# Kernel optimization log

Hardware: AMD Instinct MI355X
Metric: run time of the kernel (lower is better)

Reference implementation:

```python
import jax, jax.numpy as jnp
import numpy as np

N_NODES = 50000


def _sage_conv(x, src, dst, W_l, b_l, W_r):
    # PyG SAGEConv (aggr='mean'): out = lin_l(mean_{j in N(i)} x_j) + lin_r(x_i)
    # lin_l has bias, lin_r has no bias.
    neigh_sum = jax.ops.segment_sum(x[src], dst, num_segments=N_NODES)  # [N, F]
    deg = jax.ops.segment_sum(jnp.ones_like(dst, dtype=x.dtype), dst, num_segments=N_NODES)
    neigh_mean = neigh_sum / jnp.maximum(deg, 1.0)[:, None]
    return neigh_mean @ W_l.T + b_l + x @ W_r.T


def setup_inputs() -> dict:
    key = jax.random.key(0)
    ks = jax.random.split(key, 8)
    D, H, C = 768, 128, 4
    x = jax.random.normal(ks[0], (N_NODES, D), dtype=jnp.float32)
    edge_index = jax.random.randint(ks[1], (2, 800000), 0, N_NODES, dtype=jnp.int64)
    s1 = 1.0 / np.sqrt(D)
    s2 = 1.0 / np.sqrt(H)
    return {
        "x": x,
        "edge_index": edge_index,
        "W1_l": jax.random.uniform(ks[2], (H, D), jnp.float32, -s1, s1),
        "b1_l": jnp.zeros((H,), jnp.float32),
        "W1_r": jax.random.uniform(ks[3], (H, D), jnp.float32, -s1, s1),
        "W2_l": jax.random.uniform(ks[4], (C, H), jnp.float32, -s2, s2),
        "b2_l": jnp.zeros((C,), jnp.float32),
        "W2_r": jax.random.uniform(ks[5], (C, H), jnp.float32, -s2, s2),
    }


def reference(x, edge_index, W1_l, b1_l, W1_r, W2_l, b2_l, W2_r):
    src, dst = edge_index[0], edge_index[1]
    h = jax.nn.relu(_sage_conv(x, src, dst, W1_l, b1_l, W1_r))  # [N, H]
    out = _sage_conv(h, src, dst, W2_l, b2_l, W2_r)  # [N, C]
    return out
```

## Files before the change

### kernel.cpp

```cpp
#include <hip/hip_runtime.h>


typedef __bf16 bf16x8 __attribute__((ext_vector_type(8)));
typedef float  f32x4  __attribute__((ext_vector_type(4)));

__device__ __forceinline__ float bf16_lo(uint32_t w) {
    union { uint32_t u; float f; } c; c.u = w << 16; return c.f;
}
__device__ __forceinline__ float bf16_hi(uint32_t w) {
    union { uint32_t u; float f; } c; c.u = w & 0xffff0000u; return c.f;
}

__global__ __launch_bounds__(256)
void prep(const float* __restrict__ W1l, const float* __restrict__ W1r,
          __bf16* __restrict__ Bp, int* __restrict__ deg, int N)
{
    int i = blockIdx.x * 256 + threadIdx.x;
    if (i < N) deg[i] = 0;
    if (i < 256 * 768) {
        int col = i / 768, k = i - col * 768;
        float v = (col < 128) ? W1l[col * 768 + k] : W1r[(col - 128) * 768 + k];
        Bp[((k >> 3) << 11) + (col << 3) + (k & 7)] = (__bf16)v;
    }
}

__global__ __launch_bounds__(256)
void csr_count(const int* __restrict__ ei, int* __restrict__ deg, int E)
{
    int e = blockIdx.x * 256 + threadIdx.x;
    if (e >= E) return;
    atomicAdd(&deg[ei[E + e]], 1);
}

__global__ __launch_bounds__(1024)
void scan1(const int* __restrict__ deg, int* __restrict__ row_ptr,
           int* __restrict__ partials, int N)
{
    __shared__ int buf[1024];
    int i = blockIdx.x * 1024 + threadIdx.x;
    int v = (i < N) ? deg[i] : 0;
    int val = v;
    buf[threadIdx.x] = val;
    __syncthreads();
    for (int off = 1; off < 1024; off <<= 1) {
        int t = (threadIdx.x >= (unsigned)off) ? buf[threadIdx.x - off] : 0;
        __syncthreads();
        val += t;
        buf[threadIdx.x] = val;
        __syncthreads();
    }
    if (i < N) row_ptr[i] = val - v;
    if (threadIdx.x == 1023) partials[blockIdx.x] = val;
}

__global__ __launch_bounds__(1024)
void scan23(int* __restrict__ row_ptr, int* __restrict__ cursor,
            const int* __restrict__ partials, int N, int E, int nb)
{
    __shared__ int soff;
    int b = blockIdx.x;
    if (threadIdx.x < 64) {
        int lane = threadIdx.x;
        int v = (lane < nb) ? partials[lane] : 0;
        int s = v;
        #pragma unroll
        for (int off = 1; off < 64; off <<= 1) {
            int t = __shfl_up(s, off);
            if (lane >= off) s += t;
        }
        if (lane == b) soff = s - v;
    }
    __syncthreads();
    int off = soff;
    int i = b * 1024 + threadIdx.x;
    if (i < N) {
        int v = row_ptr[i] + off;
        row_ptr[i] = v;
        cursor[i]  = v;
    }
    if (b == 0 && threadIdx.x == 0) row_ptr[N] = E;
}

__global__ __launch_bounds__(512)
void gemm_fill(const float* __restrict__ A, const __bf16* __restrict__ Bp,
               __bf16* __restrict__ Cb, int M, int mtiles,
               const int* __restrict__ ei, int* __restrict__ cursor,
               int* __restrict__ csr_src, int E)
{
    constexpr int LDK = 136;
    __shared__ __bf16 As[64][LDK];
    const int tid = threadIdx.x;

    if ((int)blockIdx.x >= mtiles) {
        int stride = (gridDim.x - mtiles) * 512;
        for (int e = (blockIdx.x - mtiles) * 512 + tid; e < E; e += stride) {
            int src = ei[e];
            int dst = ei[E + e];
            int pos = atomicAdd(&cursor[dst], 1);
            csr_src[pos] = src;
        }
        return;
    }

    const int bm   = blockIdx.x * 64;
    const int lane = tid & 63;
    const int wave = tid >> 6;
    const int wr = wave >> 2, wc = wave & 3;
    const int l15 = lane & 15;
    const int lk  = lane >> 4;

    f32x4 acc[2][4] = {};
    float4 apref[4];

    const int arow = tid >> 3;
    const int akc  = (tid & 7) << 4;
    const __bf16* bbase = Bp + ((size_t)(wc * 64 + l15) << 3) + ((size_t)lk << 11);

    auto load_A = [&](int k0) {
        if (bm + arow < M) {
            const float* src = A + (size_t)(bm + arow) * 768 + k0 + akc;
            apref[0] = *(const float4*)src;
            apref[1] = *(const float4*)(src + 4);
            apref[2] = *(const float4*)(src + 8);
            apref[3] = *(const float4*)(src + 12);
        } else {
            apref[0] = apref[1] = apref[2] = apref[3] = make_float4(0.f, 0.f, 0.f, 0.f);
        }
    };

    load_A(0);
    for (int kt = 0; kt < 6; ++kt) {
        if (kt) __syncthreads();
        {
            bf16x8 b0, b1;
            b0[0] = (__bf16)apref[0].x; b0[1] = (__bf16)apref[0].y;
            b0[2] = (__bf16)apref[0].z; b0[3] = (__bf16)apref[0].w;
            b0[4] = (__bf16)apref[1].x; b0[5] = (__bf16)apref[1].y;
            b0[6] = (__bf16)apref[1].z; b0[7] = (__bf16)apref[1].w;
            b1[0] = (__bf16)apref[2].x; b1[1] = (__bf16)apref[2].y;
            b1[2] = (__bf16)apref[2].z; b1[3] = (__bf16)apref[2].w;
            b1[4] = (__bf16)apref[3].x; b1[5] = (__bf16)apref[3].y;
            b1[6] = (__bf16)apref[3].z; b1[7] = (__bf16)apref[3].w;
            *(bf16x8*)&As[arow][akc]     = b0;
            *(bf16x8*)&As[arow][akc + 8] = b1;
        }
        __syncthreads();
        if (kt < 5) load_A((kt + 1) * 128);

        #pragma unroll
        for (int ksp = 0; ksp < 2; ++ksp) {
            bf16x8 bcur[2][4];
            #pragma unroll
            for (int k2 = 0; k2 < 2; ++k2)
                #pragma unroll
                for (int j = 0; j < 4; ++j)
                    bcur[k2][j] = *(const bf16x8*)(bbase +
                        (((size_t)(kt * 16 + (ksp * 2 + k2) * 4) << 11) +
                         ((size_t)j << 7)));
            #pragma unroll
            for (int k2 = 0; k2 < 2; ++k2) {
                int koff = (ksp * 2 + k2) * 32 + lk * 8;
                bf16x8 af[2];
                #pragma unroll
                for (int i = 0; i < 2; ++i)
                    af[i] = *(const bf16x8*)&As[wr * 32 + i * 16 + l15][koff];
                #pragma unroll
                for (int i = 0; i < 2; ++i)
                    #pragma unroll
                    for (int j = 0; j < 4; ++j)
                        acc[i][j] = __builtin_amdgcn_mfma_f32_16x16x32_bf16(
                            af[i], bcur[k2][j], acc[i][j], 0, 0, 0);
            }
        }
    }

    #pragma unroll
    for (int i = 0; i < 2; ++i)
        #pragma unroll
        for (int j = 0; j < 4; ++j)
            #pragma unroll
            for (int v = 0; v < 4; ++v) {
                int row = bm + wr * 32 + i * 16 + lk * 4 + v;
                int col = wc * 64 + j * 16 + l15;
                if (row < M) Cb[(size_t)row * 256 + col] = (__bf16)acc[i][j][v];
            }
}

__global__ __launch_bounds__(256)
void sage1_fused(const int* __restrict__ row_ptr, const int* __restrict__ csr_src,
                 const __bf16* __restrict__ pq, const float* __restrict__ b1,
                 const float* __restrict__ W2l, const float* __restrict__ W2r,
                 float* __restrict__ r, float* __restrict__ s, int N)
{
    __shared__ float Wl[512], Wr[512];
    for (int i = threadIdx.x; i < 512; i += 256) {
        Wl[i] = W2l[i];
        Wr[i] = W2r[i];
    }
    __syncthreads();

    int wid  = threadIdx.x >> 6;
    int lane = threadIdx.x & 63;
    int g = lane >> 3;
    int l = lane & 7;
    int n = blockIdx.x * 4 + wid;
    if (n >= N) return;
    int beg = row_ptr[n], end = row_ptr[n + 1];

    float a0[8] = {}, a1[8] = {};
    for (int eb = beg; eb < end; eb += 64) {
        int cnt = min(64, end - eb);
        int id = (eb + lane < end) ? csr_src[eb + lane] : 0;
        for (int t = 0; t < cnt; t += 8) {
            int src = __shfl(id, t + g);
            if (t + g < cnt) {
                const __bf16* row = pq + (size_t)src * 256;
                uint4 w0 = *(const uint4*)(row + l * 8);
                uint4 w1 = *(const uint4*)(row + 64 + l * 8);
                a0[0] += bf16_lo(w0.x); a0[1] += bf16_hi(w0.x);
                a0[2] += bf16_lo(w0.y); a0[3] += bf16_hi(w0.y);
                a0[4] += bf16_lo(w0.z); a0[5] += bf16_hi(w0.z);
                a0[6] += bf16_lo(w0.w); a0[7] += bf16_hi(w0.w);
                a1[0] += bf16_lo(w1.x); a1[1] += bf16_hi(w1.x);
                a1[2] += bf16_lo(w1.y); a1[3] += bf16_hi(w1.y);
                a1[4] += bf16_lo(w1.z); a1[5] += bf16_hi(w1.z);
                a1[6] += bf16_lo(w1.w); a1[7] += bf16_hi(w1.w);
            }
        }
    }
    #pragma unroll
    for (int c = 0; c < 8; ++c) {
        a0[c] += __shfl_xor(a0[c], 8);  a1[c] += __shfl_xor(a1[c], 8);
        a0[c] += __shfl_xor(a0[c], 16); a1[c] += __shfl_xor(a1[c], 16);
        a0[c] += __shfl_xor(a0[c], 32); a1[c] += __shfl_xor(a1[c], 32);
    }

    float inv = 1.0f / fmaxf((float)(end - beg), 1.0f);
    const __bf16* qrow = pq + (size_t)n * 256 + 128;
    uint4  qw0 = *(const uint4*)(qrow + l * 8);
    uint4  qw1 = *(const uint4*)(qrow + 64 + l * 8);
    float4 bv00 = *(const float4*)(b1 + l * 8);
    float4 bv01 = *(const float4*)(b1 + l * 8 + 4);
    float4 bv10 = *(const float4*)(b1 + 64 + l * 8);
    float4 bv11 = *(const float4*)(b1 + 64 + l * 8 + 4);
    float h0[8], h1[8];
    h0[0] = fmaxf(a0[0] * inv + bv00.x + bf16_lo(qw0.x), 0.f);
    h0[1] = fmaxf(a0[1] * inv + bv00.y + bf16_hi(qw0.x), 0.f);
    h0[2] = fmaxf(a0[2] * inv + bv00.z + bf16_lo(qw0.y), 0.f);
    h0[3] = fmaxf(a0[3] * inv + bv00.w + bf16_hi(qw0.y), 0.f);
    h0[4] = fmaxf(a0[4] * inv + bv01.x + bf16_lo(qw0.z), 0.f);
    h0[5] = fmaxf(a0[5] * inv + bv01.y + bf16_hi(qw0.z), 0.f);
    h0[6] = fmaxf(a0[6] * inv + bv01.z + bf16_lo(qw0.w), 0.f);
    h0[7] = fmaxf(a0[7] * inv + bv01.w + bf16_hi(qw0.w), 0.f);
    h1[0] = fmaxf(a1[0] * inv + bv10.x + bf16_lo(qw1.x), 0.f);
    h1[1] = fmaxf(a1[1] * inv + bv10.y + bf16_hi(qw1.x), 0.f);
    h1[2] = fmaxf(a1[2] * inv + bv10.z + bf16_lo(qw1.y), 0.f);
    h1[3] = fmaxf(a1[3] * inv + bv10.w + bf16_hi(qw1.y), 0.f);
    h1[4] = fmaxf(a1[4] * inv + bv11.x + bf16_lo(qw1.z), 0.f);
    h1[5] = fmaxf(a1[5] * inv + bv11.y + bf16_hi(qw1.z), 0.f);
    h1[6] = fmaxf(a1[6] * inv + bv11.z + bf16_lo(qw1.w), 0.f);
    h1[7] = fmaxf(a1[7] * inv + bv11.w + bf16_hi(qw1.w), 0.f);

    float part[8];
    #pragma unroll
    for (int c = 0; c < 4; ++c) {
        float pl = 0.f, pr = 0.f;
        #pragma unroll
        for (int j = 0; j < 8; ++j) {
            pl = fmaf(h0[j], Wl[c * 128 + l * 8 + j], pl);
            pl = fmaf(h1[j], Wl[c * 128 + 64 + l * 8 + j], pl);
            pr = fmaf(h0[j], Wr[c * 128 + l * 8 + j], pr);
            pr = fmaf(h1[j], Wr[c * 128 + 64 + l * 8 + j], pr);
        }
        part[c] = pl; part[4 + c] = pr;
    }
    #pragma unroll
    for (int off = 4; off; off >>= 1)
        #pragma unroll
        for (int c = 0; c < 8; ++c)
            part[c] += __shfl_xor(part[c], off);
    if (lane == 0) {
        *(float4*)(r + (size_t)n * 4) = make_float4(part[0], part[1], part[2], part[3]);
        *(float4*)(s + (size_t)n * 4) = make_float4(part[4], part[5], part[6], part[7]);
    }
}

__global__ __launch_bounds__(256)
void sage2_gather(const int* __restrict__ row_ptr, const int* __restrict__ csr_src,
                  const float* __restrict__ r, const float* __restrict__ s,
                  const float* __restrict__ b2, float* __restrict__ out, int N)
{
    int t = blockIdx.x * 256 + threadIdx.x;
    if (t >= N * 4) return;
    int n = t >> 2, c = t & 3;
    int beg = row_ptr[n], end = row_ptr[n + 1];
    float acc = 0.f;
    for (int e = beg; e < end; ++e)
        acc += r[(size_t)csr_src[e] * 4 + c];
    out[t] = acc / fmaxf((float)(end - beg), 1.0f) + b2[c] + s[t];
}

extern "C" void kernel_launch(void* const* d_in, const int* in_sizes, int n_in,
                              void* d_out, int out_size, void* d_ws, size_t ws_size,
                              hipStream_t stream)
{
    const float* x   = (const float*)d_in[0];
    const int*   ei  = (const int*)d_in[1];
    const float* W1l = (const float*)d_in[2];
    const float* b1l = (const float*)d_in[3];
    const float* W1r = (const float*)d_in[4];
    const float* W2l = (const float*)d_in[5];
    const float* b2l = (const float*)d_in[6];
    const float* W2r = (const float*)d_in[7];
    float* out = (float*)d_out;

    const int N = in_sizes[0] / 768;
    const int E = in_sizes[1] / 2;
    const int NB = (N + 1023) / 1024;

    char* ws = (char*)d_ws;
    size_t off = 0;
    auto alloc = [&](size_t bytes) -> void* {
        void* pp = ws + off;
        off += (bytes + 255) & ~(size_t)255;
        return pp;
    };
    __bf16* pq      = (__bf16*)alloc((size_t)N * 256 * 2);
    float*  r       = (float*)alloc((size_t)N * 4 * 4);
    float*  s       = (float*)alloc((size_t)N * 4 * 4);
    __bf16* Bp      = (__bf16*)alloc((size_t)256 * 768 * 2);
    int*    deg     = (int*)alloc((size_t)N * 4);
    int*    row_ptr = (int*)alloc((size_t)(N + 1) * 4);
    int*    cursor  = (int*)alloc((size_t)N * 4);
    int*    csr_src = (int*)alloc((size_t)E * 4);
    int*    partials= (int*)alloc((size_t)64 * 4);

    prep<<<(256 * 768 + 255) / 256, 256, 0, stream>>>(W1l, W1r, Bp, deg, N);

    csr_count<<<(E + 255) / 256, 256, 0, stream>>>(ei, deg, E);
    scan1<<<NB, 1024, 0, stream>>>(deg, row_ptr, partials, N);
    scan23<<<NB, 1024, 0, stream>>>(row_ptr, cursor, partials, N, E, NB);

    const int mtiles = (N + 63) / 64;
    gemm_fill<<<mtiles + 256, 512, 0, stream>>>(x, Bp, pq, N, mtiles,
                                                ei, cursor, csr_src, E);

    sage1_fused<<<(N + 3) / 4, 256, 0, stream>>>(row_ptr, csr_src, pq, b1l,
                                                 W2l, W2r, r, s, N);

    sage2_gather<<<(N * 4 + 255) / 256, 256, 0, stream>>>(row_ptr, csr_src, r, s, b2l, out, N);
}
```

Measured before the change: 204.4 us.

## Pre-convert x to bf16 and stream GEMM A tiles via direct-to-LDS loads

x is converted to bf16 in a separate pass that is merged with the degree-count kernel. The GEMM then loads A tiles with global_load_lds into a double-buffered, XOR-swizzled LDS layout instead of staging fp32 through registers. This removes register pressure and conversion from the GEMM's inner loop and overlaps the next tile's load with MFMA work. It costs an extra full write and read of a bf16 copy of x (~77MB round trip). The padded rows of xb are left uninitialized, so the last tile reads garbage, though those rows are masked on output.

```diff
diff --git a/kernel.cpp b/kernel.cpp
--- a/kernel.cpp
+++ b/kernel.cpp
@@ -9,6 +9,12 @@
 }
 __device__ __forceinline__ float bf16_hi(uint32_t w) {
     union { uint32_t u; float f; } c; c.u = w & 0xffff0000u; return c.f;
+}
+
+__device__ __forceinline__ void load_lds16(const void* g, void* l) {
+    __builtin_amdgcn_global_load_lds(
+        (const __attribute__((address_space(1))) void*)g,
+        (__attribute__((address_space(3))) void*)l, 16, 0, 0);
 }
 
 __global__ __launch_bounds__(256)
@@ -25,11 +31,27 @@
 }
 
 __global__ __launch_bounds__(256)
-void csr_count(const int* __restrict__ ei, int* __restrict__ deg, int E)
-{
-    int e = blockIdx.x * 256 + threadIdx.x;
-    if (e >= E) return;
-    atomicAdd(&deg[ei[E + e]], 1);
+void cvt_count(const float* __restrict__ x, __bf16* __restrict__ xb, int nu8,
+               const int* __restrict__ ei, int* __restrict__ deg, int E,
+               int cblocks)
+{
+    if ((int)blockIdx.x < cblocks) {
+        int stride = cblocks * 256;
+        for (int u = blockIdx.x * 256 + threadIdx.x; u < nu8; u += stride) {
+            const float* src = x + (size_t)u * 8;
+            float4 f0 = *(const float4*)src;
+            float4 f1 = *(const float4*)(src + 4);
+            bf16x8 b;
+            b[0] = (__bf16)f0.x; b[1] = (__bf16)f0.y;
+            b[2] = (__bf16)f0.z; b[3] = (__bf16)f0.w;
+            b[4] = (__bf16)f1.x; b[5] = (__bf16)f1.y;
+            b[6] = (__bf16)f1.z; b[7] = (__bf16)f1.w;
+            *(bf16x8*)(xb + (size_t)u * 8) = b;
+        }
+    } else {
+        int e = (blockIdx.x - cblocks) * 256 + threadIdx.x;
+        if (e < E) atomicAdd(&deg[ei[E + e]], 1);
+    }
 }
 
 __global__ __launch_bounds__(1024)
@@ -82,13 +104,12 @@
 }
 
 __global__ __launch_bounds__(512)
-void gemm_fill(const float* __restrict__ A, const __bf16* __restrict__ Bp,
+void gemm_fill(const __bf16* __restrict__ xb, const __bf16* __restrict__ Bp,
                __bf16* __restrict__ Cb, int M, int mtiles,
                const int* __restrict__ ei, int* __restrict__ cursor,
                int* __restrict__ csr_src, int E)
 {
-    constexpr int LDK = 136;
-    __shared__ __bf16 As[64][LDK];
+    __shared__ __bf16 As[2][64][128];
     const int tid = threadIdx.x;
 
     if ((int)blockIdx.x >= mtiles) {
@@ -110,42 +131,25 @@
     const int lk  = lane >> 4;
 
     f32x4 acc[2][4] = {};
-    float4 apref[4];
-
-    const int arow = tid >> 3;
-    const int akc  = (tid & 7) << 4;
+
+    const int sr0 = (wave * 2 + 0) * 4 + (lane >> 4);
+    const int sr1 = (wave * 2 + 1) * 4 + (lane >> 4);
+    const int sc  = lane & 15;
+    const __bf16* g0 = xb + (size_t)(bm + sr0) * 768 + (((sc ^ (sr0 & 7))) << 3);
+    const __bf16* g1 = xb + (size_t)(bm + sr1) * 768 + (((sc ^ (sr1 & 7))) << 3);
+
     const __bf16* bbase = Bp + ((size_t)(wc * 64 + l15) << 3) + ((size_t)lk << 11);
 
-    auto load_A = [&](int k0) {
-        if (bm + arow < M) {
-            const float* src = A + (size_t)(bm + arow) * 768 + k0 + akc;
-            apref[0] = *(const float4*)src;
-            apref[1] = *(const float4*)(src + 4);
-            apref[2] = *(const float4*)(src + 8);
-            apref[3] = *(const float4*)(src + 12);
-        } else {
-            apref[0] = apref[1] = apref[2] = apref[3] = make_float4(0.f, 0.f, 0.f, 0.f);
-        }
-    };
-
-    load_A(0);
+    load_lds16(g0, &As[0][(wave * 2 + 0) * 4][0]);
+    load_lds16(g1, &As[0][(wave * 2 + 1) * 4][0]);
+    __syncthreads();
+
+    int cur = 0;
     for (int kt = 0; kt < 6; ++kt) {
-        if (kt) __syncthreads();
-        {
-            bf16x8 b0, b1;
-            b0[0] = (__bf16)apref[0].x; b0[1] = (__bf16)apref[0].y;
-            b0[2] = (__bf16)apref[0].z; b0[3] = (__bf16)apref[0].w;
-            b0[4] = (__bf16)apref[1].x; b0[5] = (__bf16)apref[1].y;
-            b0[6] = (__bf16)apref[1].z; b0[7] = (__bf16)apref[1].w;
-            b1[0] = (__bf16)apref[2].x; b1[1] = (__bf16)apref[2].y;
-            b1[2] = (__bf16)apref[2].z; b1[3] = (__bf16)apref[2].w;
-            b1[4] = (__bf16)apref[3].x; b1[5] = (__bf16)apref[3].y;
-            b1[6] = (__bf16)apref[3].z; b1[7] = (__bf16)apref[3].w;
-            *(bf16x8*)&As[arow][akc]     = b0;
-            *(bf16x8*)&As[arow][akc + 8] = b1;
-        }
-        __syncthreads();
-        if (kt < 5) load_A((kt + 1) * 128);
+        if (kt < 5) {
+            load_lds16(g0 + (kt + 1) * 128, &As[cur ^ 1][(wave * 2 + 0) * 4][0]);
+            load_lds16(g1 + (kt + 1) * 128, &As[cur ^ 1][(wave * 2 + 1) * 4][0]);
+        }
 
         #pragma unroll
         for (int ksp = 0; ksp < 2; ++ksp) {
@@ -162,8 +166,10 @@
                 int koff = (ksp * 2 + k2) * 32 + lk * 8;
                 bf16x8 af[2];
                 #pragma unroll
-                for (int i = 0; i < 2; ++i)
-                    af[i] = *(const bf16x8*)&As[wr * 32 + i * 16 + l15][koff];
+                for (int i = 0; i < 2; ++i) {
+                    int r = wr * 32 + i * 16 + l15;
+                    af[i] = *(const bf16x8*)&As[cur][r][koff ^ ((r & 7) << 3)];
+                }
                 #pragma unroll
                 for (int i = 0; i < 2; ++i)
                     #pragma unroll
@@ -172,6 +178,9 @@
                             af[i], bcur[k2][j], acc[i][j], 0, 0, 0);
             }
         }
+
+        __syncthreads();
+        cur ^= 1;
     }
 
     #pragma unroll
@@ -317,6 +326,8 @@
     const int N = in_sizes[0] / 768;
     const int E = in_sizes[1] / 2;
     const int NB = (N + 1023) / 1024;
+    const int mtiles = (N + 63) / 64;
+    const int Mpad = mtiles * 64;
 
     char* ws = (char*)d_ws;
     size_t off = 0;
@@ -325,6 +336,7 @@
         off += (bytes + 255) & ~(size_t)255;
         return pp;
     };
+    __bf16* xb      = (__bf16*)alloc((size_t)Mpad * 768 * 2);
     __bf16* pq      = (__bf16*)alloc((size_t)N * 256 * 2);
     float*  r       = (float*)alloc((size_t)N * 4 * 4);
     float*  s       = (float*)alloc((size_t)N * 4 * 4);
@@ -337,12 +349,15 @@
 
     prep<<<(256 * 768 + 255) / 256, 256, 0, stream>>>(W1l, W1r, Bp, deg, N);
 
-    csr_count<<<(E + 255) / 256, 256, 0, stream>>>(ei, deg, E);
+    const int cblocks = 2048;
+    const int nu8 = N * 96;
+    cvt_count<<<cblocks + (E + 255) / 256, 256, 0, stream>>>(
+        x, xb, nu8, ei, deg, E, cblocks);
+
     scan1<<<NB, 1024, 0, stream>>>(deg, row_ptr, partials, N);
     scan23<<<NB, 1024, 0, stream>>>(row_ptr, cursor, partials, N, E, NB);
 
-    const int mtiles = (N + 63) / 64;
-    gemm_fill<<<mtiles + 256, 512, 0, stream>>>(x, Bp, pq, N, mtiles,
+    gemm_fill<<<mtiles + 256, 512, 0, stream>>>(xb, Bp, pq, N, mtiles,
                                                 ei, cursor, csr_src, E);
 
     sage1_fused<<<(N + 3) / 4, 256, 0, stream>>>(row_ptr, csr_src, pq, b1l,
```

Result: slower. 216.7 us (+6.0%).

## Stream fp32 A tiles into LDS via async global_load_lds triple buffering

Applied to the files above, without the earlier changes.

Replaces the register-staged A-tile path (global load to registers, convert to bf16, store to LDS) with direct global-to-LDS 16-byte async loads of fp32 data into a three-stage ring buffer with XOR swizzling. The K loop now runs in 64-wide steps, with loads issued two stages ahead and a single waitcnt+barrier per step. The fp32-to-bf16 conversion moves to the point where A fragments are read from LDS. The aim is to hide global memory latency and cut register pressure and VALU work on the load path. The cost is twice the LDS bytes per element and repeated conversions during fragment reads.

```diff
diff --git a/kernel.cpp b/kernel.cpp
--- a/kernel.cpp
+++ b/kernel.cpp
@@ -9,6 +9,12 @@
 }
 __device__ __forceinline__ float bf16_hi(uint32_t w) {
     union { uint32_t u; float f; } c; c.u = w & 0xffff0000u; return c.f;
+}
+
+__device__ __forceinline__ void load_lds16(const void* g, void* l) {
+    __builtin_amdgcn_global_load_lds(
+        (const __attribute__((address_space(1))) void*)g,
+        (__attribute__((address_space(3))) void*)l, 16, 0, 0);
 }
 
 __global__ __launch_bounds__(256)
@@ -82,13 +88,12 @@
 }
 
 __global__ __launch_bounds__(512)
-void gemm_fill(const float* __restrict__ A, const __bf16* __restrict__ Bp,
+void gemm_fill(const float* __restrict__ x, const __bf16* __restrict__ Bp,
                __bf16* __restrict__ Cb, int M, int mtiles,
                const int* __restrict__ ei, int* __restrict__ cursor,
                int* __restrict__ csr_src, int E)
 {
-    constexpr int LDK = 136;
-    __shared__ __bf16 As[64][LDK];
+    __shared__ float As[3][64][64];
     const int tid = threadIdx.x;
 
     if ((int)blockIdx.x >= mtiles) {
@@ -110,67 +115,62 @@
     const int lk  = lane >> 4;
 
     f32x4 acc[2][4] = {};
-    float4 apref[4];
-
-    const int arow = tid >> 3;
-    const int akc  = (tid & 7) << 4;
+
+    const int sr0 = wave * 8 + (lane >> 4);
+    const int sr1 = wave * 8 + 4 + (lane >> 4);
+    const int sc  = lane & 15;
+    const float* g0 = x + (size_t)min(bm + sr0, M - 1) * 768 + ((sc ^ (sr0 & 7)) << 2);
+    const float* g1 = x + (size_t)min(bm + sr1, M - 1) * 768 + ((sc ^ (sr1 & 7)) << 2);
+
     const __bf16* bbase = Bp + ((size_t)(wc * 64 + l15) << 3) + ((size_t)lk << 11);
 
-    auto load_A = [&](int k0) {
-        if (bm + arow < M) {
-            const float* src = A + (size_t)(bm + arow) * 768 + k0 + akc;
-            apref[0] = *(const float4*)src;
-            apref[1] = *(const float4*)(src + 4);
-            apref[2] = *(const float4*)(src + 8);
-            apref[3] = *(const float4*)(src + 12);
-        } else {
-            apref[0] = apref[1] = apref[2] = apref[3] = make_float4(0.f, 0.f, 0.f, 0.f);
-        }
-    };
-
-    load_A(0);
-    for (int kt = 0; kt < 6; ++kt) {
-        if (kt) __syncthreads();
-        {
-            bf16x8 b0, b1;
-            b0[0] = (__bf16)apref[0].x; b0[1] = (__bf16)apref[0].y;
-            b0[2] = (__bf16)apref[0].z; b0[3] = (__bf16)apref[0].w;
-            b0[4] = (__bf16)apref[1].x; b0[5] = (__bf16)apref[1].y;
-            b0[6] = (__bf16)apref[1].z; b0[7] = (__bf16)apref[1].w;
-            b1[0] = (__bf16)apref[2].x; b1[1] = (__bf16)apref[2].y;
-            b1[2] = (__bf16)apref[2].z; b1[3] = (__bf16)apref[2].w;
-            b1[4] = (__bf16)apref[3].x; b1[5] = (__bf16)apref[3].y;
-            b1[6] = (__bf16)apref[3].z; b1[7] = (__bf16)apref[3].w;
-            *(bf16x8*)&As[arow][akc]     = b0;
-            *(bf16x8*)&As[arow][akc + 8] = b1;
-        }
-        __syncthreads();
-        if (kt < 5) load_A((kt + 1) * 128);
-
-        #pragma unroll
-        for (int ksp = 0; ksp < 2; ++ksp) {
-            bf16x8 bcur[2][4];
+    load_lds16(g0,      &As[0][wave * 8][0]);
+    load_lds16(g1,      &As[0][wave * 8 + 4][0]);
+    load_lds16(g0 + 64, &As[1][wave * 8][0]);
+    load_lds16(g1 + 64, &As[1][wave * 8 + 4][0]);
+
+    for (int kt = 0; kt < 12; ++kt) {
+        asm volatile("s_waitcnt vmcnt(2)\n\ts_barrier" ::: "memory");
+        __builtin_amdgcn_sched_barrier(0);
+        const int buf = kt % 3;
+
+        bf16x8 bcur[2][4];
+        #pragma unroll
+        for (int ks = 0; ks < 2; ++ks)
             #pragma unroll
-            for (int k2 = 0; k2 < 2; ++k2)
+            for (int j = 0; j < 4; ++j)
+                bcur[ks][j] = *(const bf16x8*)(bbase +
+                    (((size_t)(kt * 8 + ks * 4) << 11) + ((size_t)j << 7)));
+
+        if (kt < 10) {
+            const int nb = (kt + 2) % 3;
+            load_lds16(g0 + (kt + 2) * 64, &As[nb][wave * 8][0]);
+            load_lds16(g1 + (kt + 2) * 64, &As[nb][wave * 8 + 4][0]);
+        }
+
+        #pragma unroll
+        for (int ks = 0; ks < 2; ++ks) {
+            bf16x8 af[2];
+            #pragma unroll
+            for (int i = 0; i < 2; ++i) {
+                int r = wr * 32 + i * 16 + l15;
+                int sw = r & 7;
+                int c0 = (ks * 32 + lk * 8) >> 2;
+                float4 lo = *(const float4*)&As[buf][r][((c0)     ^ sw) << 2];
+                float4 hi = *(const float4*)&As[buf][r][((c0 + 1) ^ sw) << 2];
+                bf16x8 a;
+                a[0] = (__bf16)lo.x; a[1] = (__bf16)lo.y;
+                a[2] = (__bf16)lo.z; a[3] = (__bf16)lo.w;
+                a[4] = (__bf16)hi.x; a[5] = (__bf16)hi.y;
+                a[6] = (__bf16)hi.z; a[7] = (__bf16)hi.w;
+                af[i] = a;
+            }
+            #pragma unroll
+            for (int i = 0; i < 2; ++i)
                 #pragma unroll
                 for (int j = 0; j < 4; ++j)
-                    bcur[k2][j] = *(const bf16x8*)(bbase +
-                        (((size_t)(kt * 16 + (ksp * 2 + k2) * 4) << 11) +
-                         ((size_t)j << 7)));
-            #pragma unroll
-            for (int k2 = 0; k2 < 2; ++k2) {
-                int koff = (ksp * 2 + k2) * 32 + lk * 8;
-                bf16x8 af[2];
-                #pragma unroll
-                for (int i = 0; i < 2; ++i)
-                    af[i] = *(const bf16x8*)&As[wr * 32 + i * 16 + l15][koff];
-                #pragma unroll
-                for (int i = 0; i < 2; ++i)
-                    #pragma unroll
-                    for (int j = 0; j < 4; ++j)
-                        acc[i][j] = __builtin_amdgcn_mfma_f32_16x16x32_bf16(
-                            af[i], bcur[k2][j], acc[i][j], 0, 0, 0);
-            }
+                    acc[i][j] = __builtin_amdgcn_mfma_f32_16x16x32_bf16(
+                        af[i], bcur[ks][j], acc[i][j], 0, 0, 0);
         }
     }
 
@@ -317,6 +317,7 @@
     const int N = in_sizes[0] / 768;
     const int E = in_sizes[1] / 2;
     const int NB = (N + 1023) / 1024;
+    const int mtiles = (N + 63) / 64;
 
     char* ws = (char*)d_ws;
     size_t off = 0;
@@ -341,7 +342,6 @@
     scan1<<<NB, 1024, 0, stream>>>(deg, row_ptr, partials, N);
     scan23<<<NB, 1024, 0, stream>>>(row_ptr, cursor, partials, N, E, NB);
 
-    const int mtiles = (N + 63) / 64;
     gemm_fill<<<mtiles + 256, 512, 0, stream>>>(x, Bp, pq, N, mtiles,
                                                 ei, cursor, csr_src, E);
 
```

Result: no change. 203.8 us (-0.3%).
